# Kernel tuning notes

Hardware: AMD Instinct MI355X
Metric: run time of the kernel (lower is better)

## Reference

```python
import jax, jax.numpy as jnp
import numpy as np

DIM = 512
HEADS = 8
DIM_HEAD = 64
HIDDEN = HEADS * DIM_HEAD
SCALE = DIM_HEAD ** -0.5


def rmsnorm_ch(x, g):
    # F.normalize over channel dim (axis=1), then * g * sqrt(C)
    # x: [b, c, l], g: [c]
    n = jnp.maximum(jnp.linalg.norm(x, axis=1, keepdims=True), 1e-12)
    c = x.shape[1]
    return (x / n) * g[None, :, None] * (c ** 0.5)


def setup_inputs() -> dict:
    key = jax.random.key(0)
    ks = jax.random.split(key, 6)
    b, l = 8, 4096
    x = jax.random.normal(ks[0], (b, DIM, l), dtype=jnp.float32)
    g_in = jnp.ones((DIM,), dtype=jnp.float32)
    # conv1d kernel_size=1 == matmul; kaiming-ish init scale
    w_qkv = jax.random.normal(ks[1], (3 * HIDDEN, DIM), dtype=jnp.float32) * (1.0 / np.sqrt(DIM))
    w_out = jax.random.normal(ks[2], (DIM, HIDDEN), dtype=jnp.float32) * (1.0 / np.sqrt(HIDDEN))
    b_out = jax.random.normal(ks[3], (DIM,), dtype=jnp.float32) * 0.01
    g_out = jnp.ones((DIM,), dtype=jnp.float32)
    return {"x": x, "g_in": g_in, "w_qkv": w_qkv, "w_out": w_out, "b_out": b_out, "g_out": g_out}


def reference(x, g_in, w_qkv, w_out, b_out, g_out):
    b, c, l = x.shape
    residual = x
    xn = rmsnorm_ch(x, g_in)                       # [b, c, l]
    qkv = jnp.einsum('oc,bcl->bol', w_qkv, xn)     # [b, 3*hidden, l]
    q, k, v = jnp.split(qkv, 3, axis=1)            # each [b, hidden, l]
    def to_heads(t):
        return t.reshape(b, HEADS, DIM_HEAD, l)    # [b, h, d, l]
    q, k, v = to_heads(q), to_heads(k), to_heads(v)
    q = jax.nn.softmax(q, axis=2) * SCALE          # softmax over head-dim d
    k = jax.nn.softmax(k, axis=3)                  # softmax over sequence l
    context = jnp.einsum('bhdn,bhen->bhde', k, v)  # [b, h, d, e]
    out = jnp.einsum('bhde,bhdn->bhen', context, q)  # [b, h, e, l]
    out = out.reshape(b, HIDDEN, l)
    o = jnp.einsum('ch,bhl->bcl', w_out, out) + b_out[None, :, None]
    o = rmsnorm_ch(o, g_out)
    return o + residual
```

## Files before the change

kernel.cpp:

```cpp
#include <hip/hip_runtime.h>


#define BB 8
#define CC 512
#define LL 4096
#define HH 8
#define DH 64
#define TC 1536

__device__ __constant__ const float SQRT_C = 22.62741699796952f;
#define SCALE_Q 0.125f

typedef unsigned short bfr_t;
typedef __attribute__((ext_vector_type(8))) short short8;
typedef __attribute__((ext_vector_type(4))) float f32x4;
typedef __attribute__((ext_vector_type(16))) float f32x16;

__device__ __forceinline__ float bf2f(bfr_t v) {
  union { unsigned u; float f; } c; c.u = ((unsigned)v) << 16; return c.f;
}
__device__ __forceinline__ bfr_t f2bf(float f) {
  union { float f; unsigned u; } c; c.f = f;
  unsigned u = c.u + 0x7fffu + ((c.u >> 16) & 1u);
  return (bfr_t)(u >> 16);
}

__device__ __forceinline__ void load_lds16(const bfr_t* g, short* l) {
  __builtin_amdgcn_global_load_lds(
      (const __attribute__((address_space(1))) void*)g,
      (__attribute__((address_space(3))) void*)l, 16, 0, 0);
}

__global__ __launch_bounds__(256) void conv_bf16_2(
    const float* __restrict__ in1, bfr_t* __restrict__ o1, int n1,
    const float* __restrict__ in2, bfr_t* __restrict__ o2, int n2) {
  int i = blockIdx.x * 256 + threadIdx.x;
  if (i < n1) o1[i] = f2bf(in1[i]);
  int j = i - n1;
  if (j >= 0 && j < n2) o2[j] = f2bf(in2[j]);
}

__global__ __launch_bounds__(256) void fused_norm_transpose(
    const float* __restrict__ x, const float* __restrict__ g,
    bfr_t* __restrict__ xt) {
  __shared__ float tile[64][65];
  __shared__ float red[4][64];
  __shared__ float invn_s[64];
  int b = blockIdx.y, l0 = blockIdx.x * 64;
  int t = threadIdx.x, ll = t & 63, cg = t >> 6;
  const float* xb = x + (size_t)b * CC * LL + l0;
  float vals[8][16];
  float ss = 0.f;
#pragma unroll
  for (int ch = 0; ch < 8; ++ch) {
    int c0 = ch * 64;
#pragma unroll
    for (int i = 0; i < 16; ++i) {
      int c = i * 4 + cg;
      float v = xb[(size_t)(c0 + c) * LL + ll];
      vals[ch][i] = v;
      ss += v * v;
    }
  }
  red[cg][ll] = ss;
  __syncthreads();
  if (cg == 0) {
    float s = red[0][ll] + red[1][ll] + red[2][ll] + red[3][ll];
    invn_s[ll] = SQRT_C / fmaxf(sqrtf(s), 1e-12f);
  }
  __syncthreads();
  int lw = t >> 2, ccw = (t & 3) * 16;
  float iv = invn_s[lw];
#pragma unroll
  for (int ch = 0; ch < 8; ++ch) {
    int c0 = ch * 64;
#pragma unroll
    for (int i = 0; i < 16; ++i) tile[i * 4 + cg][ll] = vals[ch][i];
    __syncthreads();
    union { short s[16]; f32x4 v[2]; } pk;
#pragma unroll
    for (int u = 0; u < 16; ++u) {
      int c = ccw + u;
      pk.s[u] = (short)f2bf(tile[c][lw] * g[c0 + c] * iv);
    }
    bfr_t* dst = xt + ((size_t)b * LL + l0 + lw) * CC + c0 + ccw;
    *(f32x4*)dst = pk.v[0];
    *(f32x4*)(dst + 8) = pk.v[1];
    __syncthreads();
  }
}

__global__ __launch_bounds__(256) void gemm_bf16(
    const bfr_t* __restrict__ A, const bfr_t* __restrict__ Bt,
    bfr_t* __restrict__ Cout, const float* __restrict__ bias, int M) {
  const int K = 512;
  __shared__ short As[128 * 64];
  __shared__ short Bs[128 * 64];
  int b = blockIdx.z;
  int m0 = blockIdx.y * 128, n0 = blockIdx.x * 128;
  int t = threadIdx.x, lane = t & 63, wid = t >> 6;
  int wm = wid & 1, wn = wid >> 1;
  int l31 = lane & 31, half = lane >> 5;
  const bfr_t* Bbase = Bt + (size_t)b * LL * K;

  int lrow = lane >> 3;
  int lgran = (lane & 7) ^ lrow;
  const bfr_t* gA[4];
  const bfr_t* gB[4];
  short* lA[4];
  short* lB[4];
#pragma unroll
  for (int u = 0; u < 4; ++u) {
    int ch = wid * 4 + u;
    int row = ch * 8 + lrow;
    gA[u] = A + (size_t)(m0 + row) * K + lgran * 8;
    gB[u] = Bbase + (size_t)(n0 + row) * K + lgran * 8;
    lA[u] = As + ch * 512;
    lB[u] = Bs + ch * 512;
  }

  f32x16 acc[2][2] = {};

  for (int k0 = 0; k0 < K; k0 += 64) {
    __syncthreads();
#pragma unroll
    for (int u = 0; u < 4; ++u) {
      load_lds16(gA[u] + k0, lA[u]);
      load_lds16(gB[u] + k0, lB[u]);
    }
    __syncthreads();
#pragma unroll
    for (int kk = 0; kk < 4; ++kk) {
      short8 a[2], bq[2];
#pragma unroll
      for (int im = 0; im < 2; ++im) {
        int row = wm * 64 + im * 32 + l31;
        int gk = (kk * 2 + half) ^ (row & 7);
        a[im] = *(const short8*)&As[row * 64 + gk * 8];
      }
#pragma unroll
      for (int jn = 0; jn < 2; ++jn) {
        int row = wn * 64 + jn * 32 + l31;
        int gk = (kk * 2 + half) ^ (row & 7);
        bq[jn] = *(const short8*)&Bs[row * 64 + gk * 8];
      }
#pragma unroll
      for (int im = 0; im < 2; ++im)
#pragma unroll
        for (int jn = 0; jn < 2; ++jn)
          acc[im][jn] = __builtin_amdgcn_mfma_f32_32x32x16_bf16(
              a[im], bq[jn], acc[im][jn], 0, 0, 0);
    }
  }

  bfr_t* Cb = Cout + (size_t)b * M * LL;
#pragma unroll
  for (int im = 0; im < 2; ++im) {
#pragma unroll
    for (int reg = 0; reg < 16; ++reg) {
      int row = m0 + wm * 64 + im * 32 + (reg & 3) + 8 * (reg >> 2) + 4 * half;
      float bi = bias ? bias[row] : 0.f;
#pragma unroll
      for (int jn = 0; jn < 2; ++jn) {
        int col = n0 + wn * 64 + jn * 32 + l31;
        Cb[(size_t)row * LL + col] = f2bf(acc[im][jn][reg] + bi);
      }
    }
  }
}

__global__ __launch_bounds__(256) void kstats(const bfr_t* __restrict__ qkv,
                                              float* __restrict__ kmax,
                                              float* __restrict__ ksum) {
  __shared__ float red[256];
  int row = blockIdx.x;
  int b = row >> 9, hd = row & 511;
  const bfr_t* kr = qkv + ((size_t)b * TC + 512 + hd) * LL + (size_t)threadIdx.x * 16;
  int t = threadIdx.x;
  union { short s[16]; short8 v[2]; } u;
  u.v[0] = *(const short8*)kr;
  u.v[1] = *(const short8*)(kr + 8);
  float vals[16];
  float m = -1e30f;
#pragma unroll
  for (int i = 0; i < 16; ++i) {
    float v = bf2f((bfr_t)u.s[i]);
    vals[i] = v;
    m = fmaxf(m, v);
  }
  red[t] = m;
  __syncthreads();
  for (int s = 128; s > 0; s >>= 1) {
    if (t < s) red[t] = fmaxf(red[t], red[t + s]);
    __syncthreads();
  }
  m = red[0];
  __syncthreads();
  float ss = 0.f;
#pragma unroll
  for (int i = 0; i < 16; ++i) ss += __expf(vals[i] - m);
  red[t] = ss;
  __syncthreads();
  for (int s = 128; s > 0; s >>= 1) {
    if (t < s) red[t] += red[t + s];
    __syncthreads();
  }
  if (t == 0) { kmax[row] = m; ksum[row] = red[0]; }
}

__global__ __launch_bounds__(256) void context_mfma(
    const bfr_t* __restrict__ qkv, const float* __restrict__ kmax,
    float* __restrict__ ctx_p) {
  __shared__ float red[4][4096];
  int s = blockIdx.x, bh = blockIdx.y;
  int b = bh >> 3, h = bh & 7;
  int t = threadIdx.x, lane = t & 63, wid = t >> 6;
  int quad = lane >> 4, r = lane & 15;
  const bfr_t* kb = qkv + ((size_t)b * TC + 512 + h * 64) * LL;
  const bfr_t* vb = qkv + ((size_t)b * TC + 1024 + h * 64) * LL;
  float km[4];
#pragma unroll
  for (int i = 0; i < 4; ++i) km[i] = kmax[b * 512 + h * 64 + i * 16 + r];
  int n_base = s * 512 + wid * 128;
  f32x4 acc[4][4] = {};
#pragma unroll
  for (int ks = 0; ks < 4; ++ks) {
    int n0 = n_base + ks * 32;
    short8 af[4], bf8[4];
#pragma unroll
    for (int i = 0; i < 4; ++i) {
      union { short s[8]; short8 v8; } uk;
      uk.v8 = *(const short8*)&kb[(size_t)(i * 16 + r) * LL + n0 + quad * 8];
#pragma unroll
      for (int jj = 0; jj < 8; ++jj)
        uk.s[jj] = (short)f2bf(__expf(bf2f((bfr_t)uk.s[jj]) - km[i]));
      af[i] = uk.v8;
      bf8[i] = *(const short8*)&vb[(size_t)(i * 16 + r) * LL + n0 + quad * 8];
    }
#pragma unroll
    for (int i = 0; i < 4; ++i)
#pragma unroll
      for (int j = 0; j < 4; ++j)
        acc[i][j] = __builtin_amdgcn_mfma_f32_16x16x32_bf16(af[i], bf8[j],
                                                            acc[i][j], 0, 0, 0);
  }
#pragma unroll
  for (int i = 0; i < 4; ++i)
#pragma unroll
    for (int j = 0; j < 4; ++j)
#pragma unroll
      for (int reg = 0; reg < 4; ++reg)
        red[wid][(i * 16 + quad * 4 + reg) * 64 + j * 16 + r] = acc[i][j][reg];
  __syncthreads();
  float* out = ctx_p + ((size_t)bh * 8 + s) * 4096;
#pragma unroll
  for (int u = 0; u < 16; ++u) {
    int idx = u * 256 + t;
    out[idx] = red[0][idx] + red[1][idx] + red[2][idx] + red[3][idx];
  }
}

__global__ __launch_bounds__(256) void context_reduce(
    const float* __restrict__ ctx_p, const float* __restrict__ ksum,
    bfr_t* __restrict__ ctx_bf) {
  int bh = blockIdx.x;
  int b = bh >> 3, h = bh & 7;
  int t = threadIdx.x;
#pragma unroll
  for (int i = 0; i < 16; ++i) {
    int idx = i * 256 + t;
    int d = idx >> 6;
    float sum = 0.f;
#pragma unroll
    for (int s = 0; s < 8; ++s) sum += ctx_p[((size_t)bh * 8 + s) * 4096 + idx];
    ctx_bf[(size_t)bh * 4096 + idx] = f2bf(sum / ksum[b * 512 + h * 64 + d]);
  }
}

__global__ __launch_bounds__(256) void apply_fused(
    const bfr_t* __restrict__ qkv, const bfr_t* __restrict__ ctx_bf,
    bfr_t* __restrict__ out_t) {
  int b = blockIdx.z, h = blockIdx.y;
  int t = threadIdx.x, lane = t & 63, wid = t >> 6;
  int quad = lane >> 4, r = lane & 15;
  int n0 = blockIdx.x * 256 + wid * 64;
  const bfr_t* qb = qkv + ((size_t)b * TC + h * 64) * LL;
  const bfr_t* cb = ctx_bf + (size_t)(b * HH + h) * 4096;
  float v[4][16];
  float pm[4];
#pragma unroll
  for (int i = 0; i < 4; ++i) {
    pm[i] = -1e30f;
#pragma unroll
    for (int ks = 0; ks < 2; ++ks)
#pragma unroll
      for (int jj = 0; jj < 8; ++jj) {
        float q = bf2f(qb[(size_t)(ks * 32 + quad * 8 + jj) * LL + n0 + i * 16 + r]);
        v[i][ks * 8 + jj] = q;
        pm[i] = fmaxf(pm[i], q);
      }
  }
#pragma unroll
  for (int i = 0; i < 4; ++i) {
    pm[i] = fmaxf(pm[i], __shfl_xor(pm[i], 16, 64));
    pm[i] = fmaxf(pm[i], __shfl_xor(pm[i], 32, 64));
  }
  float psum[4];
#pragma unroll
  for (int i = 0; i < 4; ++i) {
    float s = 0.f;
#pragma unroll
    for (int u = 0; u < 16; ++u) { v[i][u] = __expf(v[i][u] - pm[i]); s += v[i][u]; }
    psum[i] = s;
  }
#pragma unroll
  for (int i = 0; i < 4; ++i) {
    psum[i] += __shfl_xor(psum[i], 16, 64);
    psum[i] += __shfl_xor(psum[i], 32, 64);
  }
  short8 af[2][4];
#pragma unroll
  for (int i = 0; i < 4; ++i) {
    float sc = SCALE_Q / psum[i];
#pragma unroll
    for (int ks = 0; ks < 2; ++ks) {
      union { short s[8]; short8 v8; } u;
#pragma unroll
      for (int jj = 0; jj < 8; ++jj) u.s[jj] = (short)f2bf(v[i][ks * 8 + jj] * sc);
      af[ks][i] = u.v8;
    }
  }
  short8 bfrag[2][4];
#pragma unroll
  for (int ks = 0; ks < 2; ++ks)
#pragma unroll
    for (int j = 0; j < 4; ++j) {
      union { short s[8]; short8 v8; } u;
#pragma unroll
      for (int jj = 0; jj < 8; ++jj)
        u.s[jj] = (short)cb[(ks * 32 + quad * 8 + jj) * 64 + j * 16 + r];
      bfrag[ks][j] = u.v8;
    }
  f32x4 acc[4][4] = {};
#pragma unroll
  for (int ks = 0; ks < 2; ++ks)
#pragma unroll
    for (int i = 0; i < 4; ++i)
#pragma unroll
      for (int j = 0; j < 4; ++j)
        acc[i][j] = __builtin_amdgcn_mfma_f32_16x16x32_bf16(af[ks][i], bfrag[ks][j],
                                                            acc[i][j], 0, 0, 0);
  bfr_t* dst = out_t + (size_t)b * LL * 512 + h * 64;
#pragma unroll
  for (int i = 0; i < 4; ++i)
#pragma unroll
    for (int reg = 0; reg < 4; ++reg) {
      int row = n0 + i * 16 + quad * 4 + reg;
#pragma unroll
      for (int j = 0; j < 4; ++j)
        dst[(size_t)row * 512 + j * 16 + r] = f2bf(acc[i][j][reg]);
    }
}

__global__ __launch_bounds__(512) void final_norm_res(
    const bfr_t* __restrict__ o, const float* __restrict__ g,
    const float* __restrict__ x, float* __restrict__ out) {
  __shared__ float red[8][64];
  __shared__ float invn[64];
  int b = blockIdx.y, l0 = blockIdx.x * 64;
  int t = threadIdx.x, ll = t & 63, cg = t >> 6;
  const bfr_t* ob = o + (size_t)b * CC * LL + l0 + ll;
  float vals[64];
  float ss = 0.f;
#pragma unroll
  for (int i = 0; i < 64; ++i) {
    int c = cg * 64 + i;
    float v = bf2f(ob[(size_t)c * LL]);
    vals[i] = v;
    ss += v * v;
  }
  red[cg][ll] = ss;
  __syncthreads();
  if (cg == 0) {
    float s = 0.f;
#pragma unroll
    for (int j = 0; j < 8; ++j) s += red[j][ll];
    invn[ll] = SQRT_C / fmaxf(sqrtf(s), 1e-12f);
  }
  __syncthreads();
  float iv = invn[ll];
  const float* xb = x + (size_t)b * CC * LL + l0 + ll;
  float* outb = out + (size_t)b * CC * LL + l0 + ll;
#pragma unroll
  for (int i = 0; i < 64; ++i) {
    int c = cg * 64 + i;
    outb[(size_t)c * LL] = vals[i] * g[c] * iv + xb[(size_t)c * LL];
  }
}

extern "C" void kernel_launch(void* const* d_in, const int* in_sizes, int n_in,
                              void* d_out, int out_size, void* d_ws,
                              size_t ws_size, hipStream_t stream) {
  const float* x     = (const float*)d_in[0];
  const float* g_in  = (const float*)d_in[1];
  const float* w_qkv = (const float*)d_in[2];
  const float* w_out = (const float*)d_in[3];
  const float* b_out = (const float*)d_in[4];
  const float* g_out = (const float*)d_in[5];
  float* out = (float*)d_out;

  char* ws = (char*)d_ws;
  const size_t off_wqkv  = 0;
  const size_t off_wout  = 1572864;
  const size_t off_kmax  = 2097152;
  const size_t off_ksum  = 2244608;
  const size_t off_ctx   = 2260992;
  const size_t off_ctxp  = 3309568;
  const size_t off_xt    = 11698176;
  const size_t off_qkv   = 45252608;
  const size_t ws_need   = 145915904;
  if (ws_size < ws_need) return;

  bfr_t* wqkv_bf = (bfr_t*)(ws + off_wqkv);
  bfr_t* wout_bf = (bfr_t*)(ws + off_wout);
  float* kmax    = (float*)(ws + off_kmax);
  float* ksum    = (float*)(ws + off_ksum);
  bfr_t* ctx_bf  = (bfr_t*)(ws + off_ctx);
  float* ctxp    = (float*)(ws + off_ctxp);
  bfr_t* xt      = (bfr_t*)(ws + off_xt);
  bfr_t* qkv     = (bfr_t*)(ws + off_qkv);
  bfr_t* o_bf    = (bfr_t*)(ws + off_qkv);

  conv_bf16_2<<<dim3((1536 * 512 + 512 * 512 + 255) / 256), 256, 0, stream>>>(
      w_qkv, wqkv_bf, 1536 * 512, w_out, wout_bf, 512 * 512);
  fused_norm_transpose<<<dim3(LL / 64, BB), 256, 0, stream>>>(x, g_in, xt);
  gemm_bf16<<<dim3(LL / 128, TC / 128, BB), 256, 0, stream>>>(wqkv_bf, xt, qkv, nullptr, TC);
  kstats<<<dim3(BB * 512), 256, 0, stream>>>(qkv, kmax, ksum);
  context_mfma<<<dim3(8, BB * HH), 256, 0, stream>>>(qkv, kmax, ctxp);
  context_reduce<<<dim3(BB * HH), 256, 0, stream>>>(ctxp, ksum, ctx_bf);
  apply_fused<<<dim3(LL / 256, HH, BB), 256, 0, stream>>>(qkv, ctx_bf, xt);
  gemm_bf16<<<dim3(LL / 128, CC / 128, BB), 256, 0, stream>>>(wout_bf, xt, o_bf, b_out, CC);
  final_norm_res<<<dim3(LL / 64, BB), 512, 0, stream>>>(o_bf, g_out, x, out);
}
```

Baseline: 310.1 us.

## Fuse k-softmax stats into context kernel, vectorize weight cast, slim final norm

Removes the separate kstats pass by computing exp(k) without max subtraction inside context_mfma and accumulating per-row partial sums, which context_reduce combines into a reciprocal normalizer. This eliminates one full read of the K tensor and a kernel launch. Dropping the max shift relies on k values being small enough that exp does not overflow, which risks numerical issues for large activations. The weight conversion kernel now handles 8 elements per thread, and final_norm_res uses 256 threads and re-reads o instead of holding 64 values in registers.

```diff
diff --git a/kernel.cpp b/kernel.cpp
--- a/kernel.cpp
+++ b/kernel.cpp
@@ -34,10 +34,21 @@
 __global__ __launch_bounds__(256) void conv_bf16_2(
     const float* __restrict__ in1, bfr_t* __restrict__ o1, int n1,
     const float* __restrict__ in2, bfr_t* __restrict__ o2, int n2) {
-  int i = blockIdx.x * 256 + threadIdx.x;
-  if (i < n1) o1[i] = f2bf(in1[i]);
-  int j = i - n1;
-  if (j >= 0 && j < n2) o2[j] = f2bf(in2[j]);
+  int i8 = (blockIdx.x * 256 + threadIdx.x) * 8;
+  const float* src;
+  bfr_t* dst;
+  if (i8 < n1) { src = in1 + i8; dst = o1 + i8; }
+  else {
+    int j8 = i8 - n1;
+    if (j8 >= n2) return;
+    src = in2 + j8; dst = o2 + j8;
+  }
+  f32x4 a = *(const f32x4*)src;
+  f32x4 b = *(const f32x4*)(src + 4);
+  union { short s[8]; f32x4 v; } pk;
+#pragma unroll
+  for (int u = 0; u < 4; ++u) { pk.s[u] = (short)f2bf(a[u]); pk.s[u + 4] = (short)f2bf(b[u]); }
+  *(f32x4*)dst = pk.v;
 }
 
 __global__ __launch_bounds__(256) void fused_norm_transpose(
@@ -169,48 +180,9 @@
   }
 }
 
-__global__ __launch_bounds__(256) void kstats(const bfr_t* __restrict__ qkv,
-                                              float* __restrict__ kmax,
-                                              float* __restrict__ ksum) {
-  __shared__ float red[256];
-  int row = blockIdx.x;
-  int b = row >> 9, hd = row & 511;
-  const bfr_t* kr = qkv + ((size_t)b * TC + 512 + hd) * LL + (size_t)threadIdx.x * 16;
-  int t = threadIdx.x;
-  union { short s[16]; short8 v[2]; } u;
-  u.v[0] = *(const short8*)kr;
-  u.v[1] = *(const short8*)(kr + 8);
-  float vals[16];
-  float m = -1e30f;
-#pragma unroll
-  for (int i = 0; i < 16; ++i) {
-    float v = bf2f((bfr_t)u.s[i]);
-    vals[i] = v;
-    m = fmaxf(m, v);
-  }
-  red[t] = m;
-  __syncthreads();
-  for (int s = 128; s > 0; s >>= 1) {
-    if (t < s) red[t] = fmaxf(red[t], red[t + s]);
-    __syncthreads();
-  }
-  m = red[0];
-  __syncthreads();
-  float ss = 0.f;
-#pragma unroll
-  for (int i = 0; i < 16; ++i) ss += __expf(vals[i] - m);
-  red[t] = ss;
-  __syncthreads();
-  for (int s = 128; s > 0; s >>= 1) {
-    if (t < s) red[t] += red[t + s];
-    __syncthreads();
-  }
-  if (t == 0) { kmax[row] = m; ksum[row] = red[0]; }
-}
-
 __global__ __launch_bounds__(256) void context_mfma(
-    const bfr_t* __restrict__ qkv, const float* __restrict__ kmax,
-    float* __restrict__ ctx_p) {
+    const bfr_t* __restrict__ qkv, float* __restrict__ ctx_p,
+    float* __restrict__ ksum_p) {
   __shared__ float red[4][4096];
   int s = blockIdx.x, bh = blockIdx.y;
   int b = bh >> 3, h = bh & 7;
@@ -218,11 +190,9 @@
   int quad = lane >> 4, r = lane & 15;
   const bfr_t* kb = qkv + ((size_t)b * TC + 512 + h * 64) * LL;
   const bfr_t* vb = qkv + ((size_t)b * TC + 1024 + h * 64) * LL;
-  float km[4];
-#pragma unroll
-  for (int i = 0; i < 4; ++i) km[i] = kmax[b * 512 + h * 64 + i * 16 + r];
   int n_base = s * 512 + wid * 128;
   f32x4 acc[4][4] = {};
+  float ps[4] = {};
 #pragma unroll
   for (int ks = 0; ks < 4; ++ks) {
     int n0 = n_base + ks * 32;
@@ -232,8 +202,11 @@
       union { short s[8]; short8 v8; } uk;
       uk.v8 = *(const short8*)&kb[(size_t)(i * 16 + r) * LL + n0 + quad * 8];
 #pragma unroll
-      for (int jj = 0; jj < 8; ++jj)
-        uk.s[jj] = (short)f2bf(__expf(bf2f((bfr_t)uk.s[jj]) - km[i]));
+      for (int jj = 0; jj < 8; ++jj) {
+        float e = __expf(bf2f((bfr_t)uk.s[jj]));
+        uk.s[jj] = (short)f2bf(e);
+        ps[i] += e;
+      }
       af[i] = uk.v8;
       bf8[i] = *(const short8*)&vb[(size_t)(i * 16 + r) * LL + n0 + quad * 8];
     }
@@ -245,6 +218,20 @@
                                                             acc[i][j], 0, 0, 0);
   }
 #pragma unroll
+  for (int i = 0; i < 4; ++i) {
+    ps[i] += __shfl_xor(ps[i], 16, 64);
+    ps[i] += __shfl_xor(ps[i], 32, 64);
+  }
+  if (quad == 0) {
+#pragma unroll
+    for (int i = 0; i < 4; ++i) red[wid][i * 16 + r] = ps[i];
+  }
+  __syncthreads();
+  if (t < 64)
+    ksum_p[((size_t)bh * 8 + s) * 64 + t] =
+        red[0][t] + red[1][t] + red[2][t] + red[3][t];
+  __syncthreads();
+#pragma unroll
   for (int i = 0; i < 4; ++i)
 #pragma unroll
     for (int j = 0; j < 4; ++j)
@@ -261,11 +248,18 @@
 }
 
 __global__ __launch_bounds__(256) void context_reduce(
-    const float* __restrict__ ctx_p, const float* __restrict__ ksum,
+    const float* __restrict__ ctx_p, const float* __restrict__ ksum_p,
     bfr_t* __restrict__ ctx_bf) {
+  __shared__ float zinv[64];
   int bh = blockIdx.x;
-  int b = bh >> 3, h = bh & 7;
   int t = threadIdx.x;
+  if (t < 64) {
+    float s = 0.f;
+#pragma unroll
+    for (int s8 = 0; s8 < 8; ++s8) s += ksum_p[((size_t)bh * 8 + s8) * 64 + t];
+    zinv[t] = 1.f / s;
+  }
+  __syncthreads();
 #pragma unroll
   for (int i = 0; i < 16; ++i) {
     int idx = i * 256 + t;
@@ -273,7 +267,7 @@
     float sum = 0.f;
 #pragma unroll
     for (int s = 0; s < 8; ++s) sum += ctx_p[((size_t)bh * 8 + s) * 4096 + idx];
-    ctx_bf[(size_t)bh * 4096 + idx] = f2bf(sum / ksum[b * 512 + h * 64 + d]);
+    ctx_bf[(size_t)bh * 4096 + idx] = f2bf(sum * zinv[d]);
   }
 }
 
@@ -362,39 +356,32 @@
     }
 }
 
-__global__ __launch_bounds__(512) void final_norm_res(
+__global__ __launch_bounds__(256) void final_norm_res(
     const bfr_t* __restrict__ o, const float* __restrict__ g,
     const float* __restrict__ x, float* __restrict__ out) {
-  __shared__ float red[8][64];
+  __shared__ float red[4][64];
   __shared__ float invn[64];
   int b = blockIdx.y, l0 = blockIdx.x * 64;
   int t = threadIdx.x, ll = t & 63, cg = t >> 6;
   const bfr_t* ob = o + (size_t)b * CC * LL + l0 + ll;
-  float vals[64];
   float ss = 0.f;
-#pragma unroll
-  for (int i = 0; i < 64; ++i) {
-    int c = cg * 64 + i;
+  for (int c = cg * 128; c < cg * 128 + 128; ++c) {
     float v = bf2f(ob[(size_t)c * LL]);
-    vals[i] = v;
     ss += v * v;
   }
   red[cg][ll] = ss;
   __syncthreads();
   if (cg == 0) {
-    float s = 0.f;
-#pragma unroll
-    for (int j = 0; j < 8; ++j) s += red[j][ll];
+    float s = red[0][ll] + red[1][ll] + red[2][ll] + red[3][ll];
     invn[ll] = SQRT_C / fmaxf(sqrtf(s), 1e-12f);
   }
   __syncthreads();
   float iv = invn[ll];
   const float* xb = x + (size_t)b * CC * LL + l0 + ll;
   float* outb = out + (size_t)b * CC * LL + l0 + ll;
-#pragma unroll
-  for (int i = 0; i < 64; ++i) {
-    int c = cg * 64 + i;
-    outb[(size_t)c * LL] = vals[i] * g[c] * iv + xb[(size_t)c * LL];
+  for (int c = cg * 128; c < cg * 128 + 128; ++c) {
+    float v = bf2f(ob[(size_t)c * LL]);
+    outb[(size_t)c * LL] = v * g[c] * iv + xb[(size_t)c * LL];
   }
 }
 
@@ -412,8 +399,7 @@
   char* ws = (char*)d_ws;
   const size_t off_wqkv  = 0;
   const size_t off_wout  = 1572864;
-  const size_t off_kmax  = 2097152;
-  const size_t off_ksum  = 2244608;
+  const size_t off_ksump = 2097152;
   const size_t off_ctx   = 2260992;
   const size_t off_ctxp  = 3309568;
   const size_t off_xt    = 11698176;
@@ -423,22 +409,20 @@
 
   bfr_t* wqkv_bf = (bfr_t*)(ws + off_wqkv);
   bfr_t* wout_bf = (bfr_t*)(ws + off_wout);
-  float* kmax    = (float*)(ws + off_kmax);
-  float* ksum    = (float*)(ws + off_ksum);
+  float* ksum_p  = (float*)(ws + off_ksump);
   bfr_t* ctx_bf  = (bfr_t*)(ws + off_ctx);
   float* ctxp    = (float*)(ws + off_ctxp);
   bfr_t* xt      = (bfr_t*)(ws + off_xt);
   bfr_t* qkv     = (bfr_t*)(ws + off_qkv);
   bfr_t* o_bf    = (bfr_t*)(ws + off_qkv);
 
-  conv_bf16_2<<<dim3((1536 * 512 + 512 * 512 + 255) / 256), 256, 0, stream>>>(
+  conv_bf16_2<<<dim3((1536 * 512 + 512 * 512) / 8 / 256), 256, 0, stream>>>(
       w_qkv, wqkv_bf, 1536 * 512, w_out, wout_bf, 512 * 512);
   fused_norm_transpose<<<dim3(LL / 64, BB), 256, 0, stream>>>(x, g_in, xt);
   gemm_bf16<<<dim3(LL / 128, TC / 128, BB), 256, 0, stream>>>(wqkv_bf, xt, qkv, nullptr, TC);
-  kstats<<<dim3(BB * 512), 256, 0, stream>>>(qkv, kmax, ksum);
-  context_mfma<<<dim3(8, BB * HH), 256, 0, stream>>>(qkv, kmax, ctxp);
-  context_reduce<<<dim3(BB * HH), 256, 0, stream>>>(ctxp, ksum, ctx_bf);
+  context_mfma<<<dim3(8, BB * HH), 256, 0, stream>>>(qkv, ctxp, ksum_p);
+  context_reduce<<<dim3(BB * HH), 256, 0, stream>>>(ctxp, ksum_p, ctx_bf);
   apply_fused<<<dim3(LL / 256, HH, BB), 256, 0, stream>>>(qkv, ctx_bf, xt);
   gemm_bf16<<<dim3(LL / 128, CC / 128, BB), 256, 0, stream>>>(wout_bf, xt, o_bf, b_out, CC);
-  final_norm_res<<<dim3(LL / 64, BB), 512, 0, stream>>>(o_bf, g_out, x, out);
-}
+  final_norm_res<<<dim3(LL / 64, BB), 256, 0, stream>>>(o_bf, g_out, x, out);
+}
```

Result: faster. 298.8 us (-3.6%).
